# Optimization experiments

Measured on AMD Instinct MI355X. Metric: run time of the kernel, lower is better.

## Reference

```python
import jax, jax.numpy as jnp
import numpy as np

T, H, I, E, K = 4096, 4096, 2048, 8, 2  # tokens, hidden, intermediate, experts, top-k


def setup_inputs() -> dict:
    key = jax.random.key(0)
    k1, k2, k3, k4, k5, k6 = jax.random.split(key, 6)
    hidden_states = jax.random.normal(k1, (T, H), dtype=jnp.float32)
    topk_weights = jax.random.uniform(k2, (T, K), dtype=jnp.float32)
    topk_ids = jax.random.randint(k3, (T, K), 0, E, dtype=jnp.int32)
    # weights stored out-features-first, matching the module: wi_*: (E, I, H), wo: (E, H, I)
    wi_0 = jax.random.normal(k4, (E, I, H), dtype=jnp.float32) * 0.02
    wi_1 = jax.random.normal(k5, (E, I, H), dtype=jnp.float32) * 0.02
    wo = jax.random.normal(k6, (E, H, I), dtype=jnp.float32) * 0.02
    return {"hidden_states": hidden_states, "topk_weights": topk_weights,
            "topk_ids": topk_ids, "wi_0": wi_0, "wi_1": wi_1, "wo": wo}


def reference(hidden_states, topk_weights, topk_ids, wi_0, wi_1, wo):
    # Equivalent math to permute -> grouped GEMM (w0,w1) -> silu*mul -> grouped GEMM (wo)
    # -> unpermute+weighted combine: out[t] = sum_k topk_w[t,k] * FFN_{e=topk_ids[t,k]}(x[t])
    n_tok = hidden_states.shape[0]
    n_exp = wi_0.shape[0]
    # dense per-token expert gates (T, E): sum of topk weights routed to each expert
    gates = jnp.zeros((n_tok, n_exp), dtype=hidden_states.dtype)
    gates = gates.at[jnp.arange(n_tok)[:, None], topk_ids].add(topk_weights)
    g = jnp.einsum('th,eih->tei', hidden_states, wi_0)   # gate proj (T,E,I)
    u = jnp.einsum('th,eih->tei', hidden_states, wi_1)   # up proj   (T,E,I)
    h = jax.nn.silu(g) * u * gates[:, :, None]           # fold combine weights in (wo is linear)
    out = jnp.einsum('tei,ehi->th', h, wo)               # down proj + combine (T,H)
    return out
```

## Files before the change

### kernel.cpp

```cpp
#include <hip/hip_runtime.h>
#include <hip/hip_bf16.h>

#define T_TOK 4096
#define H_DIM 4096
#define I_DIM 2048
#define N_EXP 8
#define TOPK  2
#define NPAIR (T_TOK*TOPK)
#define BM    128
#define BK    32
#define MAXT  (NPAIR/BM + N_EXP)
#define BM1   256
#define BN1   128
#define MAXT1 (NPAIR/BM1 + N_EXP)

#define HT_OFF   ((size_t)1 << 20)
#define W0_OFF   ((size_t)44 << 20)
#define AT_OFF   ((size_t)44 << 20)
#define WS_OFF   ((size_t)120 << 20)
#define NEED_NEW (WS_OFF + 268435456ull)

typedef __attribute__((ext_vector_type(8))) short  bf16x8;
typedef __attribute__((ext_vector_type(4))) float  f32x4v;

__device__ __forceinline__ short f2bf(float f) {
    __hip_bfloat16 h = __float2bfloat16(f);
    return __builtin_bit_cast(short, h);
}
__device__ __forceinline__ float bf2f(short s) {
    unsigned int u = ((unsigned int)(unsigned short)s) << 16;
    return __builtin_bit_cast(float, u);
}

__device__ __forceinline__ bf16x8 pack8(f32x4v a, f32x4v b) {
    bf16x8 r;
    r[0]=f2bf(a[0]); r[1]=f2bf(a[1]); r[2]=f2bf(a[2]); r[3]=f2bf(a[3]);
    r[4]=f2bf(b[0]); r[5]=f2bf(b[1]); r[6]=f2bf(b[2]); r[7]=f2bf(b[3]);
    return r;
}

__device__ __forceinline__ void load_lds16(const short* g, short* l) {
    __builtin_amdgcn_global_load_lds(
        (const __attribute__((address_space(1))) void*)g,
        (__attribute__((address_space(3))) void*)l, 16, 0, 0);
}

__global__ void cvt_kernel(const float* __restrict__ X, short* __restrict__ Xbf) {
    const size_t i = ((size_t)blockIdx.x * 256 + threadIdx.x) * 8;
    f32x4v a = *(const f32x4v*)(X + i);
    f32x4v b = *(const f32x4v*)(X + i + 4);
    *(bf16x8*)(Xbf + i) = pack8(a, b);
}

__global__ void route_kernel(const int* __restrict__ ids, const float* __restrict__ wts,
                             int* __restrict__ pair_token, float* __restrict__ pair_w,
                             int* __restrict__ tile_expert, int* __restrict__ tile_row0,
                             int* __restrict__ tile_rows,
                             int* __restrict__ t1_expert, int* __restrict__ t1_row0,
                             int* __restrict__ t1_rows)
{
    __shared__ int scn[256][N_EXP];
    const int tid = threadIdx.x;
    const int PPT = NPAIR / 256;
    const int base = tid * PPT;

    int c[N_EXP], orig[N_EXP];
    #pragma unroll
    for (int e = 0; e < N_EXP; ++e) c[e] = 0;
    for (int p = 0; p < PPT; ++p) c[ids[base + p]]++;
    #pragma unroll
    for (int e = 0; e < N_EXP; ++e) { orig[e] = c[e]; scn[tid][e] = c[e]; }
    __syncthreads();

    for (int off = 1; off < 256; off <<= 1) {
        int add[N_EXP];
        #pragma unroll
        for (int e = 0; e < N_EXP; ++e) add[e] = (tid >= off) ? scn[tid - off][e] : 0;
        __syncthreads();
        #pragma unroll
        for (int e = 0; e < N_EXP; ++e) { c[e] += add[e]; scn[tid][e] = c[e]; }
        __syncthreads();
    }

    int segs[N_EXP + 1];
    {
        int run = 0;
        #pragma unroll
        for (int e = 0; e < N_EXP; ++e) { segs[e] = run; run += scn[255][e]; }
        segs[N_EXP] = run;
    }
    int pos[N_EXP];
    #pragma unroll
    for (int e = 0; e < N_EXP; ++e) pos[e] = segs[e] + c[e] - orig[e];

    for (int p = 0; p < PPT; ++p) {
        int pp = base + p;
        int e = ids[pp];
        int q = pos[e]++;
        pair_token[q] = pp / TOPK;
        pair_w[q]     = wts[pp];
    }

    if (tid == 0) {
        int t = 0;
        for (int e = 0; e < N_EXP; ++e) {
            int s = segs[e], en = segs[e + 1];
            for (int r = s; r < en; r += BM) {
                tile_expert[t] = e; tile_row0[t] = r; tile_rows[t] = min(BM, en - r); ++t;
            }
        }
        for (; t < MAXT; ++t) { tile_expert[t] = 0; tile_row0[t] = 0; tile_rows[t] = 0; }

        t = 0;
        for (int e = 0; e < N_EXP; ++e) {
            int s = segs[e], en = segs[e + 1];
            for (int r = s; r < en; r += BM1) {
                t1_expert[t] = e; t1_row0[t] = r; t1_rows[t] = min(BM1, en - r); ++t;
            }
        }
        for (; t < MAXT1; ++t) { t1_expert[t] = 0; t1_row0[t] = 0; t1_rows[t] = 0; }
    }
}

#define PRP 132

__global__ __launch_bounds__(256) void wsprep_kernel(const float* __restrict__ Wi0,
                                                     const float* __restrict__ Wi1,
                                                     short* __restrict__ Ws) {
    const int bid = blockIdx.x;
    const int e   = bid >> 10;
    const int nt  = (bid >> 5) & 31;
    const int ktg = bid & 31;
    __shared__ short lds[128][PRP];
    const int tid = threadIdx.x;
    const float* W = (nt < 16) ? Wi0 : Wi1;
    const int jr0  = (nt & 15) * 128;
    const float* src0 = W + ((size_t)e * 2048 + jr0) * 4096 + ktg * 128;
    #pragma unroll
    for (int it = 0; it < 8; ++it) {
        int r  = it * 16 + (tid >> 4);
        int hc = (tid & 15) * 8;
        const float* s = src0 + (size_t)r * 4096 + hc;
        f32x4v a = *(const f32x4v*)s;
        f32x4v b = *(const f32x4v*)(s + 4);
        *(bf16x8*)&lds[r][hc] = pack8(a, b);
    }
    __syncthreads();
    short* dst = Ws + ((size_t)(e * 32 + nt)) * 524288 + (size_t)ktg * 2 * 8192;
    #pragma unroll
    for (int it = 0; it < 8; ++it) {
        int idx = it * 256 + tid;
        int c8  = idx >> 7;
        int r   = idx & 127;
        bf16x8 v = *(const bf16x8*)&lds[r][c8 * 8];
        *(bf16x8*)(dst + (size_t)(c8 >> 3) * 8192 + (c8 & 7) * 1024 + r * 8) = v;
    }
}

__global__ __launch_bounds__(256) void aprep128_kernel(const float* __restrict__ X,
                             const int* __restrict__ pair_token,
                             const int* __restrict__ tile_row0, const int* __restrict__ tile_rows,
                             short* __restrict__ At) {
    const int bid  = blockIdx.x;
    const int tile = bid >> 5;
    const int ktg  = bid & 31;
    const int rows = tile_rows[tile];
    if (rows == 0) return;
    const int row0 = tile_row0[tile];
    __shared__ short lds[128][PRP];
    const int tid = threadIdx.x;
    #pragma unroll
    for (int it = 0; it < 8; ++it) {
        int r  = it * 16 + (tid >> 4);
        int hc = (tid & 15) * 8;
        int tok = pair_token[row0 + min(r, rows - 1)];
        const float* s = X + (size_t)tok * 4096 + ktg * 128 + hc;
        f32x4v a = *(const f32x4v*)s;
        f32x4v b = *(const f32x4v*)(s + 4);
        *(bf16x8*)&lds[r][hc] = pack8(a, b);
    }
    __syncthreads();
    short* dst = At + (size_t)tile * 524288 + (size_t)ktg * 2 * 8192;
    #pragma unroll
    for (int it = 0; it < 8; ++it) {
        int idx = it * 256 + tid;
        int c8  = idx >> 7;
        int r   = idx & 127;
        bf16x8 v = *(const bf16x8*)&lds[r][c8 * 8];
        *(bf16x8*)(dst + (size_t)(c8 >> 3) * 8192 + (c8 & 7) * 1024 + r * 8) = v;
    }
}

__global__ __launch_bounds__(256) void woprep2_kernel(const float* __restrict__ W, short* __restrict__ Wt) {
    const int bid = blockIdx.x;
    const int e   = bid >> 9;
    const int hb  = (bid >> 4) & 31;
    const int ktg = bid & 15;
    __shared__ short lds[128][PRP];
    const int tid = threadIdx.x;
    const float* src0 = W + ((size_t)(e * 4096 + hb * 128)) * 2048 + ktg * 128;
    #pragma unroll
    for (int it = 0; it < 8; ++it) {
        int r  = it * 16 + (tid >> 4);
        int hc = (tid & 15) * 8;
        const float* s = src0 + (size_t)r * 2048 + hc;
        f32x4v a = *(const f32x4v*)s;
        f32x4v b = *(const f32x4v*)(s + 4);
        *(bf16x8*)&lds[r][hc] = pack8(a, b);
    }
    __syncthreads();
    short* dst = Wt + ((size_t)(e * 32 + hb)) * 262144 + (size_t)ktg * 2 * 8192;
    #pragma unroll
    for (int it = 0; it < 8; ++it) {
        int idx = it * 256 + tid;
        int c8  = idx >> 7;
        int r   = idx & 127;
        bf16x8 v = *(const bf16x8*)&lds[r][c8 * 8];
        *(bf16x8*)(dst + (size_t)(c8 >> 3) * 8192 + (c8 & 7) * 1024 + r * 8) = v;
    }
}

__global__ __launch_bounds__(256, 3) void gemm1s_kernel(
    const short* __restrict__ At,
    const short* __restrict__ Ws,
    const int* __restrict__ tile_expert, const int* __restrict__ tile_row0,
    const int* __restrict__ tile_rows,
    short* __restrict__ GU)
{
    const int b   = blockIdx.x;
    const int l   = (b & 7) * 288 + (b >> 3);
    const int tile  = l >> 5;
    const int n0idx = l & 31;
    const int rows = tile_rows[tile];
    if (rows == 0) return;
    const int e    = tile_expert[tile];
    const int row0 = tile_row0[tile];

    __shared__ short sAB[2048 * 8];

    const int tid  = threadIdx.x;
    const int lane = tid & 63;
    const int w    = tid >> 6;

    const short* aT = At + (size_t)tile * 524288;
    const short* bT = Ws + ((size_t)e * 32 + n0idx) * 524288;

    const int wr = w >> 1, wc = w & 1;
    const int frow = lane & 15, fsel = lane >> 4;

    f32x4v acc[4][4];
    #pragma unroll
    for (int mf = 0; mf < 4; ++mf)
        #pragma unroll
        for (int nf = 0; nf < 4; ++nf) acc[mf][nf] = (f32x4v)0.f;

    const int KT = H_DIM / 64;
    for (int kt = 0; kt < KT; ++kt) {
        __syncthreads();
        {
            const size_t ko = (size_t)kt * 8192;
            #pragma unroll
            for (int i = 0; i < 4; ++i) {
                load_lds16(aT + ko + (size_t)tid * 8 + i * 2048,
                           &sAB[(i * 256 + w * 64) * 8]);
                load_lds16(bT + ko + (size_t)tid * 8 + i * 2048,
                           &sAB[((1024 + i * 256 + w * 64)) * 8]);
            }
        }
        __syncthreads();

        #pragma unroll
        for (int h = 0; h < 2; ++h) {
            const int c = h * 4 + fsel;
            bf16x8 af[4];
            #pragma unroll
            for (int mf = 0; mf < 4; ++mf)
                af[mf] = *(const bf16x8*)&sAB[(c * 128 + wr * 64 + mf * 16 + frow) * 8];
            #pragma unroll
            for (int nf = 0; nf < 4; ++nf) {
                bf16x8 bf = *(const bf16x8*)&sAB[(1024 + c * 128 + wc * 64 + nf * 16 + frow) * 8];
                #pragma unroll
                for (int mf = 0; mf < 4; ++mf)
                    acc[mf][nf] = __builtin_amdgcn_mfma_f32_16x16x32_bf16(af[mf], bf, acc[mf][nf], 0, 0, 0);
            }
        }
    }

    const int r4 = fsel * 4;
    #pragma unroll
    for (int mf = 0; mf < 4; ++mf)
        #pragma unroll
        for (int nf = 0; nf < 4; ++nf) {
            const int col = n0idx * 128 + wc * 64 + nf * 16 + frow;
            #pragma unroll
            for (int j = 0; j < 4; ++j) {
                int rr = wr * 64 + mf * 16 + r4 + j;
                if (rr < rows)
                    GU[(size_t)(row0 + rr) * 4096 + col] = f2bf(acc[mf][nf][j]);
            }
        }
}

__global__ __launch_bounds__(256) void act_kernel(
    const short* __restrict__ GU,
    const float* __restrict__ pair_w,
    const int* __restrict__ tile_row0, const int* __restrict__ tile_rows,
    short* __restrict__ Ht)
{
    const int bid  = blockIdx.x;
    const int tile = bid >> 7;
    const int r    = bid & 127;
    const int rows = tile_rows[tile];
    if (r >= rows) return;
    const int p    = tile_row0[tile] + r;
    const float pw = pair_w[p];
    const int tid  = threadIdx.x;

    const short* g8p = GU + (size_t)p * 4096 + tid * 8;
    bf16x8 g8 = *(const bf16x8*)g8p;
    bf16x8 u8 = *(const bf16x8*)(g8p + 2048);
    bf16x8 o;
    #pragma unroll
    for (int k = 0; k < 8; ++k) {
        float g = bf2f(g8[k]);
        float u = bf2f(u8[k]);
        float sig = 1.f / (1.f + __expf(-g));
        o[k] = f2bf(g * sig * u * pw);
    }
    *(bf16x8*)(Ht + (size_t)tile * 262144 + (size_t)(tid >> 3) * 8192
               + (tid & 7) * 1024 + r * 8) = o;
}

__global__ __launch_bounds__(256, 3) void gemm2s_kernel(
    const short* __restrict__ Ht,
    const short* __restrict__ Wot,
    const int* __restrict__ pair_token,
    const int* __restrict__ tile_expert, const int* __restrict__ tile_row0,
    const int* __restrict__ tile_rows,
    float* __restrict__ out)
{
    const int b   = blockIdx.x;
    const int l   = (b & 7) * 288 + (b >> 3);
    const int tile  = l >> 5;
    const int n0idx = l & 31;
    const int rows = tile_rows[tile];
    if (rows == 0) return;
    const int e    = tile_expert[tile];
    const int row0 = tile_row0[tile];

    __shared__ short sAB[2048 * 8];
    __shared__ int   sTok[128];

    const int tid  = threadIdx.x;
    const int lane = tid & 63;
    const int w    = tid >> 6;

    if (tid < 128) sTok[tid] = pair_token[row0 + min(tid, rows - 1)];
    __syncthreads();

    const short* aT = Ht  + (size_t)tile * 262144;
    const short* bT = Wot + ((size_t)e * 32 + n0idx) * 262144;

    const int wr = w >> 1, wc = w & 1;
    const int frow = lane & 15, fsel = lane >> 4;

    f32x4v acc[4][4];
    #pragma unroll
    for (int mf = 0; mf < 4; ++mf)
        #pragma unroll
        for (int nf = 0; nf < 4; ++nf) acc[mf][nf] = (f32x4v)0.f;

    const int KT = I_DIM / 64;
    for (int kt = 0; kt < KT; ++kt) {
        __syncthreads();
        {
            const size_t ko = (size_t)kt * 8192;
            #pragma unroll
            for (int i = 0; i < 4; ++i) {
                load_lds16(aT + ko + (size_t)tid * 8 + i * 2048,
                           &sAB[(i * 256 + w * 64) * 8]);
                load_lds16(bT + ko + (size_t)tid * 8 + i * 2048,
                           &sAB[((1024 + i * 256 + w * 64)) * 8]);
            }
        }
        __syncthreads();

        #pragma unroll
        for (int h = 0; h < 2; ++h) {
            const int c = h * 4 + fsel;
            bf16x8 af[4];
            #pragma unroll
            for (int mf = 0; mf < 4; ++mf)
                af[mf] = *(const bf16x8*)&sAB[(c * 128 + wr * 64 + mf * 16 + frow) * 8];
            #pragma unroll
            for (int nf = 0; nf < 4; ++nf) {
                bf16x8 bf = *(const bf16x8*)&sAB[(1024 + c * 128 + wc * 64 + nf * 16 + frow) * 8];
                #pragma unroll
                for (int mf = 0; mf < 4; ++mf)
                    acc[mf][nf] = __builtin_amdgcn_mfma_f32_16x16x32_bf16(af[mf], bf, acc[mf][nf], 0, 0, 0);
            }
        }
    }

    const int r4 = fsel * 4;
    #pragma unroll
    for (int mf = 0; mf < 4; ++mf)
        #pragma unroll
        for (int nf = 0; nf < 4; ++nf) {
            const int col = n0idx * 128 + wc * 64 + nf * 16 + frow;
            #pragma unroll
            for (int j = 0; j < 4; ++j) {
                int rr = wr * 64 + mf * 16 + r4 + j;
                if (rr < rows)
                    atomicAdd(out + (size_t)sTok[rr] * H_DIM + col, acc[mf][nf][j]);
            }
        }
}

__global__ __launch_bounds__(512, 2) void gemm1_kernel(
    const short* __restrict__ Xbf, const float* __restrict__ Wi0, const float* __restrict__ Wi1,
    const int* __restrict__ pair_token, const float* __restrict__ pair_w,
    const int* __restrict__ t1_expert, const int* __restrict__ t1_row0, const int* __restrict__ t1_rows,
    short* __restrict__ Hbuf)
{
    const int tile = blockIdx.x;
    const int rows = t1_rows[tile];
    if (rows == 0) return;
    const int e    = t1_expert[tile];
    const int row0 = t1_row0[tile];
    const int n0   = blockIdx.y * BN1;

    __shared__ short sA [2][BM1][64];
    __shared__ short sB0[2][BN1][64 + 8];
    __shared__ short sB1[2][BN1][64 + 8];
    __shared__ int   sTok[BM1];
    __shared__ float sPw [BM1];

    const int tid  = threadIdx.x;
    const int lane = tid & 63;
    const int w    = tid >> 6;

    if (tid < BM1) {
        int tr = min(tid, rows - 1);
        sTok[tid] = pair_token[row0 + tr];
        sPw[tid]  = (tid < rows) ? pair_w[row0 + tid] : 0.f;
    }
    __syncthreads();

    const short* aSrc[4];
    #pragma unroll
    for (int i = 0; i < 4; ++i) {
        int r = w * 32 + i * 8 + (lane >> 3);
        int j = lane & 7;
        aSrc[i] = Xbf + (size_t)sTok[r] * H_DIM + ((j ^ (r & 7)) * 8);
    }

    const int brow = tid >> 2;
    const int bq   = tid & 3;
    const size_t wboff = ((size_t)e * I_DIM + (n0 + brow)) * H_DIM + bq * 16;
    const float* b0p = Wi0 + wboff;
    const float* b1p = Wi1 + wboff;

    const int wr   = w >> 1;
    const int wc   = w & 1;
    const int frow = lane & 15;
    const int fsel = lane >> 4;

    f32x4v accg[4][4], accu[4][4];
    #pragma unroll
    for (int mf = 0; mf < 4; ++mf)
        #pragma unroll
        for (int nf = 0; nf < 4; ++nf) { accg[mf][nf] = (f32x4v)0.f; accu[mf][nf] = (f32x4v)0.f; }

    f32x4v rb0[4], rb1[4];

    #pragma unroll
    for (int i = 0; i < 4; ++i)
        load_lds16(aSrc[i], &sA[0][w * 32 + i * 8][0]);
    #pragma unroll
    for (int i = 0; i < 4; ++i) { rb0[i] = *(const f32x4v*)(b0p + i * 4); rb1[i] = *(const f32x4v*)(b1p + i * 4); }
    {
        short* d0 = &sB0[0][brow][bq * 16];
        *(bf16x8*)d0       = pack8(rb0[0], rb0[1]);
        *(bf16x8*)(d0 + 8) = pack8(rb0[2], rb0[3]);
        short* d1 = &sB1[0][brow][bq * 16];
        *(bf16x8*)d1       = pack8(rb1[0], rb1[1]);
        *(bf16x8*)(d1 + 8) = pack8(rb1[2], rb1[3]);
    }
    __syncthreads();

    const int KT = H_DIM / 64;
    for (int kt = 0; kt < KT; ++kt) {
        const int cur = kt & 1, nxt = cur ^ 1;
        if (kt + 1 < KT) {
            #pragma unroll
            for (int i = 0; i < 4; ++i)
                load_lds16(aSrc[i] + (kt + 1) * 64, &sA[nxt][w * 32 + i * 8][0]);
            const float* p0 = b0p + (kt + 1) * 64;
            const float* p1 = b1p + (kt + 1) * 64;
            #pragma unroll
            for (int i = 0; i < 4; ++i) { rb0[i] = *(const f32x4v*)(p0 + i * 4); rb1[i] = *(const f32x4v*)(p1 + i * 4); }
        }
        #pragma unroll
        for (int h = 0; h < 2; ++h) {
            bf16x8 af[4], b0f[4], b1f[4];
            #pragma unroll
            for (int mf = 0; mf < 4; ++mf) {
                int ar = wr * 64 + mf * 16 + frow;
                int c  = (h * 4 + fsel) ^ (ar & 7);
                af[mf] = *(const bf16x8*)((const char*)&sA[cur][0][0] + ar * 128 + c * 16);
            }
            #pragma unroll
            for (int nf = 0; nf < 4; ++nf) {
                int br = wc * 64 + nf * 16 + frow;
                b0f[nf] = *(const bf16x8*)&sB0[cur][br][h * 32 + fsel * 8];
                b1f[nf] = *(const bf16x8*)&sB1[cur][br][h * 32 + fsel * 8];
            }
            #pragma unroll
            for (int nf = 0; nf < 4; ++nf)
                #pragma unroll
                for (int mf = 0; mf < 4; ++mf) {
                    accg[mf][nf] = __builtin_amdgcn_mfma_f32_16x16x32_bf16(af[mf], b0f[nf], accg[mf][nf], 0, 0, 0);
                    accu[mf][nf] = __builtin_amdgcn_mfma_f32_16x16x32_bf16(af[mf], b1f[nf], accu[mf][nf], 0, 0, 0);
                }
        }
        if (kt + 1 < KT) {
            short* d0 = &sB0[nxt][brow][bq * 16];
            *(bf16x8*)d0       = pack8(rb0[0], rb0[1]);
            *(bf16x8*)(d0 + 8) = pack8(rb0[2], rb0[3]);
            short* d1 = &sB1[nxt][brow][bq * 16];
            *(bf16x8*)d1       = pack8(rb1[0], rb1[1]);
            *(bf16x8*)(d1 + 8) = pack8(rb1[2], rb1[3]);
        }
        __syncthreads();
    }

    const int r4 = fsel * 4;
    #pragma unroll
    for (int mf = 0; mf < 4; ++mf)
        #pragma unroll
        for (int nf = 0; nf < 4; ++nf)
            #pragma unroll
            for (int j = 0; j < 4; ++j) {
                int rr = wr * 64 + mf * 16 + r4 + j;
                if (rr < rows) {
                    float g = accg[mf][nf][j];
                    float u = accu[mf][nf][j];
                    float sig = 1.f / (1.f + __expf(-g));
                    float v = g * sig * u * sPw[rr];
                    int col = n0 + wc * 64 + nf * 16 + frow;
                    Hbuf[(size_t)(row0 + rr) * I_DIM + col] = f2bf(v);
                }
            }
}

__global__ __launch_bounds__(256, 2) void gemm2_kernel(
    const short* __restrict__ Hbuf, const float* __restrict__ Wo,
    const int* __restrict__ pair_token,
    const int* __restrict__ tile_expert, const int* __restrict__ tile_row0,
    const int* __restrict__ tile_rows,
    float* __restrict__ out)
{
    const int tile = blockIdx.x;
    const int rows = tile_rows[tile];
    if (rows == 0) return;
    const int e    = tile_expert[tile];
    const int row0 = tile_row0[tile];
    const int n0   = blockIdx.y * 256;

    __shared__ short sA[BM][BK + 8];
    __shared__ short sB[256][BK + 8];
    __shared__ int   sTok[BM];

    const int tid = threadIdx.x;
    if (tid < BM) sTok[tid] = pair_token[row0 + min(tid, rows - 1)];
    __syncthreads();

    const int srow  = tid >> 1;
    const int shalf = tid & 1;

    const short* aptr = Hbuf + (size_t)(row0 + min(srow, rows - 1)) * I_DIM + shalf * 16;
    const float* bptrA = Wo + ((size_t)e * H_DIM + (n0 + srow))       * I_DIM + shalf * 16;
    const float* bptrB = Wo + ((size_t)e * H_DIM + (n0 + srow + 128)) * I_DIM + shalf * 16;

    bf16x8 ra[2];
    f32x4v rbA[4], rbB[4];
    f32x4v acc[4][8];
    #pragma unroll
    for (int mf = 0; mf < 4; ++mf)
        #pragma unroll
        for (int nf = 0; nf < 8; ++nf) acc[mf][nf] = (f32x4v)0.f;

    const int lane = tid & 63;
    const int wid  = tid >> 6;
    const int wr   = wid >> 1;
    const int wc   = wid & 1;
    const int frow = lane & 15;
    const int fk   = (lane >> 4) * 8;

    ra[0] = *(const bf16x8*)(aptr);
    ra[1] = *(const bf16x8*)(aptr + 8);
    #pragma unroll
    for (int i = 0; i < 4; ++i) { rbA[i] = *(const f32x4v*)(bptrA + i * 4); rbB[i] = *(const f32x4v*)(bptrB + i * 4); }

    const int KT = I_DIM / BK;
    for (int kt = 0; kt < KT; ++kt) {
        __syncthreads();
        *(bf16x8*)&sA[srow][shalf * 16]           = ra[0];
        *(bf16x8*)&sA[srow][shalf * 16 + 8]       = ra[1];
        *(bf16x8*)&sB[srow][shalf * 16]           = pack8(rbA[0], rbA[1]);
        *(bf16x8*)&sB[srow][shalf * 16 + 8]       = pack8(rbA[2], rbA[3]);
        *(bf16x8*)&sB[srow + 128][shalf * 16]     = pack8(rbB[0], rbB[1]);
        *(bf16x8*)&sB[srow + 128][shalf * 16 + 8] = pack8(rbB[2], rbB[3]);
        __syncthreads();

        if (kt + 1 < KT) {
            const int k = (kt + 1) * BK;
            ra[0] = *(const bf16x8*)(aptr + k);
            ra[1] = *(const bf16x8*)(aptr + k + 8);
            #pragma unroll
            for (int i = 0; i < 4; ++i) { rbA[i] = *(const f32x4v*)(bptrA + k + i * 4); rbB[i] = *(const f32x4v*)(bptrB + k + i * 4); }
        }

        bf16x8 af[4];
        #pragma unroll
        for (int mf = 0; mf < 4; ++mf)
            af[mf] = *(const bf16x8*)&sA[wr * 64 + mf * 16 + frow][fk];
        #pragma unroll
        for (int nf = 0; nf < 8; ++nf) {
            bf16x8 bfv = *(const bf16x8*)&sB[wc * 128 + nf * 16 + frow][fk];
            #pragma unroll
            for (int mf = 0; mf < 4; ++mf)
                acc[mf][nf] = __builtin_amdgcn_mfma_f32_16x16x32_bf16(af[mf], bfv, acc[mf][nf], 0, 0, 0);
        }
    }

    const int r4 = (lane >> 4) * 4;
    #pragma unroll
    for (int mf = 0; mf < 4; ++mf)
        #pragma unroll
        for (int nf = 0; nf < 8; ++nf)
            #pragma unroll
            for (int j = 0; j < 4; ++j) {
                int rr = wr * 64 + mf * 16 + r4 + j;
                if (rr < rows) {
                    int col = n0 + wc * 128 + nf * 16 + (lane & 15);
                    atomicAdd(out + (size_t)sTok[rr] * H_DIM + col, acc[mf][nf][j]);
                }
            }
}

extern "C" void kernel_launch(void* const* d_in, const int* in_sizes, int n_in,
                              void* d_out, int out_size, void* d_ws, size_t ws_size,
                              hipStream_t stream)
{
    (void)in_sizes; (void)n_in;
    const float* X     = (const float*)d_in[0];
    const float* topw  = (const float*)d_in[1];
    const int*   topid = (const int*)d_in[2];
    const float* Wi0   = (const float*)d_in[3];
    const float* Wi1   = (const float*)d_in[4];
    const float* Wo    = (const float*)d_in[5];
    float* out = (float*)d_out;

    char* ws = (char*)d_ws;
    int*   pair_token  = (int*)ws;
    float* pair_w      = (float*)(ws + NPAIR * 4);
    int*   tile_expert = (int*)(ws + NPAIR * 8);
    int*   tile_row0   = tile_expert + MAXT;
    int*   tile_rows   = tile_row0 + MAXT;
    int*   t1_expert   = tile_rows + MAXT;
    int*   t1_row0     = t1_expert + MAXT1;
    int*   t1_rows     = t1_row0 + MAXT1;

    route_kernel<<<1, 256, 0, stream>>>(topid, topw, pair_token, pair_w,
                                        tile_expert, tile_row0, tile_rows,
                                        t1_expert, t1_row0, t1_rows);

    if (ws_size >= NEED_NEW) {
        short* Ht  = (short*)(ws + HT_OFF);
        short* At  = (short*)(ws + AT_OFF);
        short* Ws  = (short*)(ws + WS_OFF);
        short* Wot = (short*)(ws + W0_OFF);
        short* GU  = (short*)d_out;

        aprep128_kernel<<<2304, 256, 0, stream>>>(X, pair_token, tile_row0, tile_rows, At);
        wsprep_kernel<<<8192, 256, 0, stream>>>(Wi0, Wi1, Ws);

        gemm1s_kernel<<<2304, 256, 0, stream>>>(
            At, Ws, tile_expert, tile_row0, tile_rows, GU);

        act_kernel<<<MAXT * 128, 256, 0, stream>>>(GU, pair_w, tile_row0, tile_rows, Ht);

        hipMemsetAsync(d_out, 0, (size_t)out_size * sizeof(float), stream);

        woprep2_kernel<<<4096, 256, 0, stream>>>(Wo, Wot);

        gemm2s_kernel<<<2304, 256, 0, stream>>>(
            Ht, Wot, pair_token, tile_expert, tile_row0, tile_rows, out);
    } else {
        short* Hbuf = (short*)(ws + (1 << 20));
        short* Xbf  = (short*)d_out;

        cvt_kernel<<<T_TOK * H_DIM / (256 * 8), 256, 0, stream>>>(X, Xbf);

        gemm1_kernel<<<dim3(MAXT1, I_DIM / BN1), 512, 0, stream>>>(
            Xbf, Wi0, Wi1, pair_token, pair_w, t1_expert, t1_row0, t1_rows, Hbuf);

        hipMemsetAsync(d_out, 0, (size_t)out_size * sizeof(float), stream);

        gemm2_kernel<<<dim3(MAXT, H_DIM / 256), 256, 0, stream>>>(
            Hbuf, Wo, pair_token, tile_expert, tile_row0, tile_rows, out);
    }
}
```

Before: 884.9 us.

## Fuse SiLU-gating activation into first grouped GEMM epilogue via interleaved gate/up weights

The weight-prep kernel now packs 64 gate rows and 64 up rows into each 128-column B tile, so one GEMM block holds matching gate and up outputs. The first GEMM switches to a 4x1 warp layout where each warp covers all 128 columns, computes silu(g)*u*pair_weight in the epilogue, and writes directly to the Ht layout. This removes the separate activation kernel and the round-trip of the bf16 GU intermediate through global memory. In exchange, each tile produces half as many useful output columns per B load, and the epilogue does scattered 2-byte stores.

```diff
diff --git a/kernel.cpp b/kernel.cpp
--- a/kernel.cpp
+++ b/kernel.cpp
@@ -133,14 +133,14 @@
     const int ktg = bid & 31;
     __shared__ short lds[128][PRP];
     const int tid = threadIdx.x;
-    const float* W = (nt < 16) ? Wi0 : Wi1;
-    const int jr0  = (nt & 15) * 128;
-    const float* src0 = W + ((size_t)e * 2048 + jr0) * 4096 + ktg * 128;
+    const float* srcG = Wi0 + ((size_t)e * 2048 + nt * 64) * 4096 + ktg * 128;
+    const float* srcU = Wi1 + ((size_t)e * 2048 + nt * 64) * 4096 + ktg * 128;
     #pragma unroll
     for (int it = 0; it < 8; ++it) {
         int r  = it * 16 + (tid >> 4);
         int hc = (tid & 15) * 8;
-        const float* s = src0 + (size_t)r * 4096 + hc;
+        const float* s = (r < 64) ? (srcG + (size_t)r * 4096 + hc)
+                                  : (srcU + (size_t)(r - 64) * 4096 + hc);
         f32x4v a = *(const f32x4v*)s;
         f32x4v b = *(const f32x4v*)(s + 4);
         *(bf16x8*)&lds[r][hc] = pack8(a, b);
@@ -220,12 +220,13 @@
     }
 }
 
-__global__ __launch_bounds__(256, 3) void gemm1s_kernel(
+__global__ __launch_bounds__(256, 3) void gemm1f_kernel(
     const short* __restrict__ At,
     const short* __restrict__ Ws,
+    const float* __restrict__ pair_w,
     const int* __restrict__ tile_expert, const int* __restrict__ tile_row0,
     const int* __restrict__ tile_rows,
-    short* __restrict__ GU)
+    short* __restrict__ Ht)
 {
     const int b   = blockIdx.x;
     const int l   = (b & 7) * 288 + (b >> 3);
@@ -237,22 +238,25 @@
     const int row0 = tile_row0[tile];
 
     __shared__ short sAB[2048 * 8];
+    __shared__ float sPw[128];
 
     const int tid  = threadIdx.x;
     const int lane = tid & 63;
     const int w    = tid >> 6;
 
+    if (tid < 128) sPw[tid] = (tid < rows) ? pair_w[row0 + tid] : 0.f;
+    __syncthreads();
+
     const short* aT = At + (size_t)tile * 524288;
     const short* bT = Ws + ((size_t)e * 32 + n0idx) * 524288;
 
-    const int wr = w >> 1, wc = w & 1;
     const int frow = lane & 15, fsel = lane >> 4;
 
-    f32x4v acc[4][4];
-    #pragma unroll
-    for (int mf = 0; mf < 4; ++mf)
-        #pragma unroll
-        for (int nf = 0; nf < 4; ++nf) acc[mf][nf] = (f32x4v)0.f;
+    f32x4v acc[2][8];
+    #pragma unroll
+    for (int mf = 0; mf < 2; ++mf)
+        #pragma unroll
+        for (int nf = 0; nf < 8; ++nf) acc[mf][nf] = (f32x4v)0.f;
 
     const int KT = H_DIM / 64;
     for (int kt = 0; kt < KT; ++kt) {
@@ -272,63 +276,38 @@
         #pragma unroll
         for (int h = 0; h < 2; ++h) {
             const int c = h * 4 + fsel;
-            bf16x8 af[4];
-            #pragma unroll
-            for (int mf = 0; mf < 4; ++mf)
-                af[mf] = *(const bf16x8*)&sAB[(c * 128 + wr * 64 + mf * 16 + frow) * 8];
-            #pragma unroll
-            for (int nf = 0; nf < 4; ++nf) {
-                bf16x8 bf = *(const bf16x8*)&sAB[(1024 + c * 128 + wc * 64 + nf * 16 + frow) * 8];
+            bf16x8 af[2];
+            #pragma unroll
+            for (int mf = 0; mf < 2; ++mf)
+                af[mf] = *(const bf16x8*)&sAB[(c * 128 + w * 32 + mf * 16 + frow) * 8];
+            #pragma unroll
+            for (int nf = 0; nf < 8; ++nf) {
+                bf16x8 bf = *(const bf16x8*)&sAB[(1024 + c * 128 + nf * 16 + frow) * 8];
                 #pragma unroll
-                for (int mf = 0; mf < 4; ++mf)
+                for (int mf = 0; mf < 2; ++mf)
                     acc[mf][nf] = __builtin_amdgcn_mfma_f32_16x16x32_bf16(af[mf], bf, acc[mf][nf], 0, 0, 0);
             }
         }
     }
 
-    const int r4 = fsel * 4;
-    #pragma unroll
-    for (int mf = 0; mf < 4; ++mf)
-        #pragma unroll
-        for (int nf = 0; nf < 4; ++nf) {
-            const int col = n0idx * 128 + wc * 64 + nf * 16 + frow;
+    #pragma unroll
+    for (int mf = 0; mf < 2; ++mf)
+        #pragma unroll
+        for (int nfg = 0; nfg < 4; ++nfg) {
+            const int c_g = n0idx * 64 + nfg * 16 + frow;
+            const size_t cb = (size_t)tile * 262144 + (size_t)(c_g >> 6) * 8192
+                            + ((c_g >> 3) & 7) * 1024 + (c_g & 7);
             #pragma unroll
             for (int j = 0; j < 4; ++j) {
-                int rr = wr * 64 + mf * 16 + r4 + j;
-                if (rr < rows)
-                    GU[(size_t)(row0 + rr) * 4096 + col] = f2bf(acc[mf][nf][j]);
-            }
-        }
-}
-
-__global__ __launch_bounds__(256) void act_kernel(
-    const short* __restrict__ GU,
-    const float* __restrict__ pair_w,
-    const int* __restrict__ tile_row0, const int* __restrict__ tile_rows,
-    short* __restrict__ Ht)
-{
-    const int bid  = blockIdx.x;
-    const int tile = bid >> 7;
-    const int r    = bid & 127;
-    const int rows = tile_rows[tile];
-    if (r >= rows) return;
-    const int p    = tile_row0[tile] + r;
-    const float pw = pair_w[p];
-    const int tid  = threadIdx.x;
-
-    const short* g8p = GU + (size_t)p * 4096 + tid * 8;
-    bf16x8 g8 = *(const bf16x8*)g8p;
-    bf16x8 u8 = *(const bf16x8*)(g8p + 2048);
-    bf16x8 o;
-    #pragma unroll
-    for (int k = 0; k < 8; ++k) {
-        float g = bf2f(g8[k]);
-        float u = bf2f(u8[k]);
-        float sig = 1.f / (1.f + __expf(-g));
-        o[k] = f2bf(g * sig * u * pw);
-    }
-    *(bf16x8*)(Ht + (size_t)tile * 262144 + (size_t)(tid >> 3) * 8192
-               + (tid & 7) * 1024 + r * 8) = o;
+                int row = w * 32 + mf * 16 + fsel * 4 + j;
+                if (row < rows) {
+                    float g = acc[mf][nfg][j];
+                    float u = acc[mf][nfg + 4][j];
+                    float sig = 1.f / (1.f + __expf(-g));
+                    Ht[cb + (size_t)row * 8] = f2bf(g * sig * u * sPw[row]);
+                }
+            }
+        }
 }
 
 __global__ __launch_bounds__(256, 3) void gemm2s_kernel(
@@ -682,15 +661,12 @@
         short* At  = (short*)(ws + AT_OFF);
         short* Ws  = (short*)(ws + WS_OFF);
         short* Wot = (short*)(ws + W0_OFF);
-        short* GU  = (short*)d_out;
 
         aprep128_kernel<<<2304, 256, 0, stream>>>(X, pair_token, tile_row0, tile_rows, At);
         wsprep_kernel<<<8192, 256, 0, stream>>>(Wi0, Wi1, Ws);
 
-        gemm1s_kernel<<<2304, 256, 0, stream>>>(
-            At, Ws, tile_expert, tile_row0, tile_rows, GU);
-
-        act_kernel<<<MAXT * 128, 256, 0, stream>>>(GU, pair_w, tile_row0, tile_rows, Ht);
+        gemm1f_kernel<<<2304, 256, 0, stream>>>(
+            At, Ws, pair_w, tile_expert, tile_row0, tile_rows, Ht);
 
         hipMemsetAsync(d_out, 0, (size_t)out_size * sizeof(float), stream);
 
```

Measured after the change: 825.7 us. -6.7%, faster.
